# Optimization experiments

Hardware: AMD Instinct MI355X
Metric: run time of the kernel (lower is better)

Reference implementation:

```python
import jax, jax.numpy as jnp
import numpy as np

G, N, H, OUT, L = 16, 96, 128, 1, 3
DEG = 16
E = G * N * DEG


def setup_inputs() -> dict:
    key = jax.random.key(0)
    ks = iter(jax.random.split(key, 64))
    x = jax.random.randint(next(ks), (G * N, 9), 0, 2)
    edge_attr = jax.random.randint(next(ks), (E, 3), 0, 2)
    # edges grouped per graph (matches PyG batching); global node ids
    edge_graph = jnp.repeat(jnp.arange(G), E // G)
    edge_src = edge_graph * N + jax.random.randint(next(ks), (E,), 0, N)
    edge_dst = edge_graph * N + jax.random.randint(next(ks), (E,), 0, N)

    def lin(shape, fan_in):
        return jax.random.normal(next(ks), shape, jnp.float32) / np.sqrt(fan_in)

    return dict(
        x=x, edge_attr=edge_attr, edge_src=edge_src, edge_dst=edge_dst,
        num_graphs=G, max_nodes=N,
        atom_tables=jax.random.normal(next(ks), (9, 119, H)) * 0.02,
        bond_tables=jax.random.normal(next(ks), (3, 6, H)) * 0.02,
        W_m1=lin((L, 2, 2 * H, H), 2 * H), b_m1=jnp.zeros((L, 2, H)),
        W_m2=lin((L, 2, 2 * H, H), 2 * H), b_m2=jnp.zeros((L, 2, H)),
        W_me=lin((L, 2, H, H), H), b_me=jnp.zeros((L, 2, H)),
        W_mg=lin((L, 2, H, H), H), b_mg=jnp.zeros((L, 2, H)),
        W_mlp1=lin((L, 2, H, H), H), b_mlp1=jnp.zeros((L, 2, H)),
        W_mlp2=lin((L, 2, H, H), H), b_mlp2=jnp.zeros((L, 2, H)),
        W_o1=lin((L, 2, 2 * H, H), 2 * H), b_o1=jnp.zeros((L, 2, H)),
        W_o2=lin((L, 2, H, H), H), b_o2=jnp.zeros((L, 2, H)),
        ln_g=jnp.ones((L, 2, H)), ln_b=jnp.zeros((L, 2, H)),
        W_red=lin((L, 2 * H, H), 2 * H), b_red=jnp.zeros((L, H)),
        W_p1=lin((H, H), H), b_p1=jnp.zeros((H,)),
        W_p2=lin((H, OUT), H), b_p2=jnp.zeros((OUT,)),
    )


def _forward(x, edge_attr, edge_src, edge_dst, num_graphs, max_nodes,
             atom_tables, bond_tables, W_m1, b_m1, W_m2, b_m2, W_me, b_me,
             W_mg, b_mg, W_mlp1, b_mlp1, W_mlp2, b_mlp2, W_o1, b_o1,
             W_o2, b_o2, ln_g, ln_b, W_red, b_red, W_p1, b_p1, W_p2, b_p2):
    Hd = atom_tables.shape[-1]
    # OGB encoders: sum of per-column embeddings
    node_fts = atom_tables[jnp.arange(9)[:, None], x.T].sum(0)          # [G*N, H]
    edge_fts = bond_tables[jnp.arange(3)[:, None], edge_attr.T].sum(0)  # [E, H]
    node = node_fts.reshape(num_graphs, max_nodes, Hd)                  # to_dense_batch (equal-size graphs)
    # per-graph localization of global edge ids (== subtracting per-graph min)
    g = edge_src // max_nodes
    li = edge_src % max_nodes
    lj = edge_dst % max_nodes
    edge_dense = jnp.zeros((num_graphs, max_nodes, max_nodes, Hd),
                           node.dtype).at[g, li, lj].set(edge_fts)      # [G,N,N,H]
    graph_fts = jnp.zeros((num_graphs, Hd), node.dtype)
    hidden = jnp.zeros_like(node)
    for i in range(W_m1.shape[0]):
        outs = []
        for s in range(2):  # random / pretrained streams
            z = jnp.concatenate([node, hidden], -1)                     # [G,N,2H]
            msg1 = z @ W_m1[i, s] + b_m1[i, s]                          # [G,N,H]
            msg2 = z @ W_m2[i, s] + b_m2[i, s]
            msge = edge_dense @ W_me[i, s] + b_me[i, s]                 # [G,N,N,H]
            msgg = graph_fts @ W_mg[i, s] + b_mg[i, s]                  # [G,H]
            msgs = (msg1[:, None, :, :] + msg2[:, :, None, :]
                    + msge + msgg[:, None, None, :])
            m = jax.nn.relu(msgs)
            m = jax.nn.relu(m @ W_mlp1[i, s] + b_mlp1[i, s])
            msgs = m @ W_mlp2[i, s] + b_mlp2[i, s]
            # adj_mat is all ones -> masked max reduces to plain max over senders
            msgs = msgs.max(axis=1)                                     # [G,N,H]
            ret = z @ W_o1[i, s] + b_o1[i, s] + msgs @ W_o2[i, s] + b_o2[i, s]
            ret = jax.nn.relu(ret)
            mu = ret.mean(-1, keepdims=True)
            var = jnp.mean((ret - mu) ** 2, -1, keepdims=True)
            ret = (ret - mu) / jnp.sqrt(var + 1e-5) * ln_g[i, s] + ln_b[i, s]
            outs.append(ret)
        hidden = jnp.concatenate(outs, -1) @ W_red[i] + b_red[i]
    emb = hidden.mean(1)                                                # [G,H]
    h = jax.nn.relu(emb @ W_p1 + b_p1)
    return h @ W_p2 + b_p2                                              # [G,OUT]


def reference(x, edge_attr, edge_src, edge_dst, num_graphs, max_nodes,
              atom_tables, bond_tables, W_m1, b_m1, W_m2, b_m2, W_me, b_me,
              W_mg, b_mg, W_mlp1, b_mlp1, W_mlp2, b_mlp2, W_o1, b_o1,
              W_o2, b_o2, ln_g, ln_b, W_red, b_red, W_p1, b_p1, W_p2, b_p2):
    return _forward(x, edge_attr, edge_src, edge_dst, num_graphs, max_nodes,
                    atom_tables, bond_tables, W_m1, b_m1, W_m2, b_m2, W_me, b_me,
                    W_mg, b_mg, W_mlp1, b_mlp1, W_mlp2, b_mlp2, W_o1, b_o1,
                    W_o2, b_o2, ln_g, ln_b, W_red, b_red, W_p1, b_p1, W_p2, b_p2)
```

## Files before the change

### kernel.cpp

```cpp
#include <hip/hip_runtime.h>
#include <cstddef>

typedef _Float16 f16;
typedef f16 f16x8 __attribute__((ext_vector_type(8)));
typedef f16 f16x4 __attribute__((ext_vector_type(4)));
typedef float f32x4 __attribute__((ext_vector_type(4)));

constexpr int NG    = 16;
constexpr int NNODE = 96;
constexpr int TOTN  = 1536;
constexpr int HD    = 128;
constexpr int NEDGE = 24576;
constexpr int NLAY  = 3;
constexpr int NREG  = NG * 6 * 4;
constexpr int EMCAP = 128;
constexpr int EMSTR = 136;

__device__ __forceinline__ f32x4 mfma16(f16x8 a, f16x8 b, f32x4 c) {
    return __builtin_amdgcn_mfma_f32_16x16x32_f16(a, b, c, 0, 0, 0);
}

__global__ void k_embed_nodes(const int* x, const float* atab, f16* zA) {
    const int v = blockIdx.x, h = threadIdx.x;
    float s = 0.f;
    for (int c = 0; c < 9; ++c)
        s += atab[((size_t)(c * 119 + x[v * 9 + c])) * HD + h];
    const size_t base = ((size_t)(v >> 4) * 32);
    zA[((base + (h >> 3)) * 16 + (v & 15)) * 8 + (h & 7)] = (f16)s;
    zA[((base + 16 + (h >> 3)) * 16 + (v & 15)) * 8 + (h & 7)] = (f16)0.f;
}

__global__ void k_embed_edges(const int* ea, const float* btab, f16* eftsA) {
    const int e = blockIdx.x, h = threadIdx.x;
    float s = 0.f;
    for (int c = 0; c < 3; ++c)
        s += btab[((size_t)(c * 6 + ea[e * 3 + c])) * HD + h];
    eftsA[(((size_t)(e >> 4) * 16 + (h >> 3)) * 16 + (e & 15)) * 8 + (h & 7)] = (f16)s;
}

__global__ void k_init(int* winner, int* winner2, int* eperm, int* cnt) {
    const int idx = blockIdx.x * 256 + threadIdx.x;
    if (idx < NG * NNODE * NNODE) {
        winner[idx] = -1;
        winner2[idx] = -1;
    }
    if (idx < NEDGE) eperm[idx] = -1;
    if (idx < NREG) cnt[idx] = 0;
}

__global__ void k_winner(const int* esrc, const int* edst, int* winner) {
    const int e = blockIdx.x * 256 + threadIdx.x;
    const int sg = esrc[e];
    const int g = sg / NNODE;
    const int li = sg - g * NNODE;
    const int lj = edst[e] - g * NNODE;
    atomicMax(&winner[((size_t)g * NNODE + li) * NNODE + lj], e);
}

__device__ __forceinline__ int region_of(int idx) {
    const int b = idx / (NNODE * NNODE);
    const int r = idx - b * NNODE * NNODE;
    const int i = r / NNODE, j = r - (r / NNODE) * NNODE;
    return b * 24 + (j >> 4) * 4 + (i / 24);
}

__global__ void k_count(const int* winner, int* cnt) {
    const int idx = blockIdx.x * 256 + threadIdx.x;
    if (idx < NG * NNODE * NNODE && winner[idx] >= 0)
        atomicAdd(&cnt[region_of(idx)], 1);
}

__global__ void k_scan(const int* cnt, int* base, int* base0) {
    __shared__ int tmp[NREG];
    const int t = threadIdx.x;
    tmp[t] = cnt[t];
    __syncthreads();
    for (int off = 1; off < NREG; off <<= 1) {
        int v = (t >= off) ? tmp[t - off] : 0;
        __syncthreads();
        tmp[t] += v;
        __syncthreads();
    }
    const int ex = tmp[t] - cnt[t];
    base[t] = ex;
    base0[t] = ex;
}

__global__ void k_assign(const int* winner, int* base, int* winner2, int* eperm) {
    const int idx = blockIdx.x * 256 + threadIdx.x;
    if (idx >= NG * NNODE * NNODE) return;
    const int e = winner[idx];
    if (e >= 0) {
        const int p = atomicAdd(&base[region_of(idx)], 1);
        winner2[idx] = p;
        eperm[e] = p;
    }
}

__global__ void k_wswz(const float* Wm1, const float* Wm2, const float* Wo1,
                       const float* Wred, const float* Wo2, const float* W1,
                       const float* W2, const float* We,
                       f16* sm1, f16* sm2, f16* so1, f16* sred, f16* so2,
                       f16* s1, f16* s2, f16* sme) {
    const int idx = blockIdx.x * 256 + threadIdx.x;
    const int S256 = 6 * 256 * 128;
    const int SRED = 3 * 256 * 128;
    const int S128 = 6 * 128 * 128;
    const float* src;
    f16* dst;
    int rel, sh;
    if (idx < S256)                   { src = Wm1;  dst = sm1;  rel = idx;              sh = 15; }
    else if (idx < 2 * S256)          { src = Wm2;  dst = sm2;  rel = idx - S256;       sh = 15; }
    else if (idx < 3 * S256)          { src = Wo1;  dst = so1;  rel = idx - 2 * S256;   sh = 15; }
    else if (idx < 3 * S256 + SRED)   { src = Wred; dst = sred; rel = idx - 3 * S256;   sh = 15; }
    else if (idx < 3 * S256 + SRED + S128)
        { src = Wo2; dst = so2; rel = idx - 3 * S256 - SRED; sh = 14; }
    else if (idx < 3 * S256 + SRED + 2 * S128)
        { src = W1;  dst = s1;  rel = idx - 3 * S256 - SRED - S128; sh = 14; }
    else if (idx < 3 * S256 + SRED + 3 * S128)
        { src = W2;  dst = s2;  rel = idx - 3 * S256 - SRED - 2 * S128; sh = 14; }
    else if (idx < 3 * S256 + SRED + 4 * S128)
        { src = We;  dst = sme; rel = idx - 3 * S256 - SRED - 3 * S128; sh = 14; }
    else return;
    const int mat = rel >> sh;
    const int r2 = rel & ((1 << sh) - 1);
    const int k = r2 >> 7, n = r2 & 127;
    dst[(size_t)mat * (1 << sh) + (((k >> 3) * 128 + n) << 3) + (k & 7)] = (f16)src[rel];
}

__global__ __launch_bounds__(256) void k_ngemm(
    const f16* __restrict__ zA,
    const f16* __restrict__ sm1, const f16* __restrict__ sm2, const f16* __restrict__ so1,
    const float* __restrict__ bm1, const float* __restrict__ bm2,
    const float* __restrict__ bme, const float* __restrict__ bmg,
    const float* __restrict__ bo1,
    float* __restrict__ msg1, float* __restrict__ msg2, float* __restrict__ o1buf,
    int layer) {
    const int tid = threadIdx.x, lane = tid & 63, w = tid >> 6;
    const int mr = lane & 15, q = lane >> 4;
    const int t0 = blockIdx.x;
    const int wh = blockIdx.y >> 1, s = blockIdx.y & 1, ls = layer * 2 + s;
    const f16* B;
    float* out;
    float bias[8];
    if (wh == 0) {
        B = sm1 + (size_t)ls * 32768; out = msg1 + (size_t)s * TOTN * HD;
        for (int nt = 0; nt < 8; ++nt) {
            const int col = nt * 16 + mr;
            bias[nt] = bm1[ls * HD + col] + bme[ls * HD + col] + bmg[ls * HD + col];
        }
    } else if (wh == 1) {
        B = sm2 + (size_t)ls * 32768; out = msg2 + (size_t)s * TOTN * HD;
        for (int nt = 0; nt < 8; ++nt) bias[nt] = bm2[ls * HD + nt * 16 + mr];
    } else {
        B = so1 + (size_t)ls * 32768; out = o1buf + (size_t)s * TOTN * HD;
        for (int nt = 0; nt < 8; ++nt) bias[nt] = bo1[ls * HD + nt * 16 + mr];
    }
    const size_t tIdx = (size_t)t0 * 4 + w;
    f32x4 acc[8];
#pragma unroll
    for (int nt = 0; nt < 8; ++nt) acc[nt] = (f32x4){0.f, 0.f, 0.f, 0.f};
#pragma unroll
    for (int kt = 0; kt < 8; ++kt) {
        const int kq = kt * 4 + q;
        f16x8 a = *(const f16x8*)&zA[((tIdx * 32 + kq) * 16 + mr) * 8];
        const f16* bp = B + ((size_t)kq * HD) * 8;
#pragma unroll
        for (int nt = 0; nt < 8; ++nt) {
            f16x8 bv = *(const f16x8*)(bp + (nt * 16 + mr) * 8);
            acc[nt] = mfma16(a, bv, acc[nt]);
        }
    }
#pragma unroll
    for (int nt = 0; nt < 8; ++nt) {
        const int col = nt * 16 + mr;
#pragma unroll
        for (int r = 0; r < 4; ++r) {
            const int row = t0 * 64 + w * 16 + q * 4 + r;
            out[(size_t)row * HD + col] = acc[nt][r] + bias[nt];
        }
    }
}

__global__ __launch_bounds__(256) void k_egemm(
    const f16* __restrict__ eftsA, const f16* __restrict__ sme,
    const int* __restrict__ eperm, f16* __restrict__ emsgP) {
    const int tid = threadIdx.x, lane = tid & 63, w = tid >> 6;
    const int mr = lane & 15, q = lane >> 4;
    const int ls = blockIdx.y;
    const f16* B = sme + (size_t)ls * 16384;
    f32x4 acc[2][8];
#pragma unroll
    for (int mt = 0; mt < 2; ++mt)
#pragma unroll
        for (int nt = 0; nt < 8; ++nt) acc[mt][nt] = (f32x4){0.f, 0.f, 0.f, 0.f};
#pragma unroll
    for (int kt = 0; kt < 4; ++kt) {
        const int kq = kt * 4 + q;
        f16x8 a0 = *(const f16x8*)&eftsA[(((size_t)(blockIdx.x * 8 + 2 * w + 0) * 16 + kq) * 16 + mr) * 8];
        f16x8 a1 = *(const f16x8*)&eftsA[(((size_t)(blockIdx.x * 8 + 2 * w + 1) * 16 + kq) * 16 + mr) * 8];
        const f16* bp = B + ((size_t)kq * HD) * 8;
#pragma unroll
        for (int nt = 0; nt < 8; ++nt) {
            f16x8 bv = *(const f16x8*)(bp + (nt * 16 + mr) * 8);
            acc[0][nt] = mfma16(a0, bv, acc[0][nt]);
            acc[1][nt] = mfma16(a1, bv, acc[1][nt]);
        }
    }
#pragma unroll
    for (int mt = 0; mt < 2; ++mt) {
        const int ebase = blockIdx.x * 128 + (2 * w + mt) * 16 + q * 4;
#pragma unroll
        for (int r = 0; r < 4; ++r) {
            const int p = eperm[ebase + r];
            if (p < 0) continue;
            f16* orow = emsgP + ((size_t)ls * NEDGE + p) * HD;
#pragma unroll
            for (int nt = 0; nt < 8; ++nt)
                orow[nt * 16 + mr] = (f16)acc[mt][nt][r];
        }
    }
}

__global__ __launch_bounds__(256) void k_pairs(
    const float* __restrict__ msg1, const float* __restrict__ msg2,
    const f16* __restrict__ emsgP, const int* __restrict__ winner2,
    const int* __restrict__ cnt0, const int* __restrict__ base0,
    const f16* __restrict__ w1s, const float* __restrict__ bmlp1,
    const f16* __restrict__ w2s, const float* __restrict__ bmlp2,
    float* __restrict__ maxpart, int layer) {
    __shared__ __align__(16) f16 M2s[24 * 128];
    __shared__ __align__(16) f16 Qb[128 * 128];
    __shared__ __align__(16) f16 EMs[EMCAP * EMSTR];
    const int tid = threadIdx.x, lane = tid & 63, w = tid >> 6;
    const int mr = lane & 15, q = lane >> 4;
    const int jt = blockIdx.x, b = blockIdx.y, zz = blockIdx.z;
    const int cp = zz >> 1, s = zz & 1, ls = layer * 2 + s;
    const int j0 = jt * 16, i0 = cp * 24;
    const f16* EM = emsgP + (size_t)ls * NEDGE * HD;
    const f16* W1 = w1s + (size_t)ls * HD * HD;
    const f16* W2 = w2s + (size_t)ls * HD * HD;
    const int reg = b * 24 + jt * 4 + cp;
    const int rbase = base0[reg];
    const int rcnt = cnt0[reg];
    {
        const int lim = (rcnt < EMCAP ? rcnt : EMCAP) * 16;
        for (int idx = tid; idx < lim; idx += 256) {
            const int row = idx >> 4, seg = idx & 15;
            *(f16x8*)&EMs[row * EMSTR + seg * 8] =
                *(const f16x8*)&EM[((size_t)(rbase + row)) * HD + seg * 8];
        }
    }
    for (int idx = tid * 4; idx < 24 * 128; idx += 1024) {
        const int row = idx >> 7, col = idx & 127;
        float4 v = *(const float4*)&msg2[((size_t)s * TOTN + b * NNODE + i0 + row) * HD + col];
        f16x4 h;
        h[0] = (f16)v.x; h[1] = (f16)v.y; h[2] = (f16)v.z; h[3] = (f16)v.w;
        *(f16x4*)&M2s[idx] = h;
    }
    f16x8 m1f[4];
    {
        const float* m1p = msg1 + ((size_t)s * TOTN + b * NNODE + j0 + mr) * HD;
#pragma unroll
        for (int kt = 0; kt < 4; ++kt) {
            float4 p0 = *(const float4*)(m1p + kt * 32 + q * 8);
            float4 p1 = *(const float4*)(m1p + kt * 32 + q * 8 + 4);
            m1f[kt][0] = (f16)p0.x; m1f[kt][1] = (f16)p0.y;
            m1f[kt][2] = (f16)p0.z; m1f[kt][3] = (f16)p0.w;
            m1f[kt][4] = (f16)p1.x; m1f[kt][5] = (f16)p1.y;
            m1f[kt][6] = (f16)p1.z; m1f[kt][7] = (f16)p1.w;
        }
    }
    f16x8 Bf1[4][2], Bf2[4][2];
#pragma unroll
    for (int kt = 0; kt < 4; ++kt)
#pragma unroll
        for (int ntl = 0; ntl < 2; ++ntl) {
            const size_t off = ((size_t)(kt * 4 + q) * 128 + (2 * w + ntl) * 16 + mr) * 8;
            Bf1[kt][ntl] = *(const f16x8*)(W1 + off);
            Bf2[kt][ntl] = *(const f16x8*)(W2 + off);
        }
    float b1v[2], b2v[2];
#pragma unroll
    for (int ntl = 0; ntl < 2; ++ntl) {
        const int col = (2 * w + ntl) * 16 + mr;
        b1v[ntl] = bmlp1[ls * HD + col];
        b2v[ntl] = bmlp2[ls * HD + col];
    }
    float maxr[2][4];
#pragma unroll
    for (int ntl = 0; ntl < 2; ++ntl)
#pragma unroll
        for (int r = 0; r < 4; ++r) maxr[ntl][r] = -3.402823466e38f;
    __syncthreads();

    for (int it = 0; it < 3; ++it) {
        const int ibase = i0 + it * 8;
        int wv[8];
#pragma unroll
        for (int mt = 0; mt < 8; ++mt)
            wv[mt] = winner2[((size_t)b * NNODE + ibase + mt) * NNODE + j0 + mr];
        f32x4 acc[8][2];
#pragma unroll
        for (int mt = 0; mt < 8; ++mt)
#pragma unroll
            for (int ntl = 0; ntl < 2; ++ntl) acc[mt][ntl] = (f32x4){0.f, 0.f, 0.f, 0.f};
#pragma unroll
        for (int kt = 0; kt < 4; ++kt) {
            const int ko = kt * 32 + q * 8;
#pragma unroll
            for (int mt = 0; mt < 8; ++mt) {
                f16x8 m2v = *(const f16x8*)&M2s[(it * 8 + mt) * 128 + ko];
                f16x8 av = m1f[kt] + m2v;
                if (wv[mt] >= 0) {
                    const int lp = wv[mt] - rbase;
                    const f16* ep = (lp < EMCAP) ? &EMs[lp * EMSTR + ko]
                                                 : &EM[(size_t)wv[mt] * HD + ko];
                    f16x8 ev = *(const f16x8*)ep;
                    av = av + ev;
                }
#pragma unroll
                for (int u = 0; u < 8; ++u)
                    av[u] = av[u] > (f16)0.f ? av[u] : (f16)0.f;
                acc[mt][0] = mfma16(av, Bf1[kt][0], acc[mt][0]);
                acc[mt][1] = mfma16(av, Bf1[kt][1], acc[mt][1]);
            }
        }
#pragma unroll
        for (int mt = 0; mt < 8; ++mt)
#pragma unroll
            for (int ntl = 0; ntl < 2; ++ntl) {
                const int col = (2 * w + ntl) * 16 + mr;
                const int kg = col >> 3, kj = col & 7;
#pragma unroll
                for (int r = 0; r < 4; ++r) {
                    float v = fmaxf(acc[mt][ntl][r] + b1v[ntl], 0.f);
                    Qb[((mt * 16 + kg) * 16 + q * 4 + r) * 8 + kj] = (f16)v;
                }
            }
        __syncthreads();
#pragma unroll
        for (int mt = 0; mt < 8; ++mt)
#pragma unroll
            for (int ntl = 0; ntl < 2; ++ntl) acc[mt][ntl] = (f32x4){0.f, 0.f, 0.f, 0.f};
#pragma unroll
        for (int kt = 0; kt < 4; ++kt) {
#pragma unroll
            for (int mt = 0; mt < 8; ++mt) {
                f16x8 a = *(const f16x8*)&Qb[((mt * 16 + kt * 4 + q) * 16 + mr) * 8];
                acc[mt][0] = mfma16(a, Bf2[kt][0], acc[mt][0]);
                acc[mt][1] = mfma16(a, Bf2[kt][1], acc[mt][1]);
            }
        }
#pragma unroll
        for (int ntl = 0; ntl < 2; ++ntl)
#pragma unroll
            for (int r = 0; r < 4; ++r) {
                float m0 = acc[0][ntl][r];
#pragma unroll
                for (int mt = 1; mt < 8; ++mt) m0 = fmaxf(m0, acc[mt][ntl][r]);
                maxr[ntl][r] = fmaxf(maxr[ntl][r], m0 + b2v[ntl]);
            }
        __syncthreads();
    }
#pragma unroll
    for (int ntl = 0; ntl < 2; ++ntl) {
        const int col = (2 * w + ntl) * 16 + mr;
#pragma unroll
        for (int r = 0; r < 4; ++r) {
            const int j = j0 + q * 4 + r;
            maxpart[((size_t)zz * TOTN + b * NNODE + j) * HD + col] = maxr[ntl][r];
        }
    }
}

__global__ __launch_bounds__(256) void k_pr(
    const float* __restrict__ maxpart, const float* __restrict__ o1buf,
    const f16* __restrict__ so2, const float* __restrict__ bo2,
    const float* __restrict__ lng, const float* __restrict__ lnb,
    const f16* __restrict__ sred, const float* __restrict__ bred,
    float* __restrict__ hiddenf, f16* __restrict__ zA, int layer) {
    __shared__ __align__(16) f16 Af[16384];
    const int tid = threadIdx.x, lane = tid & 63, w = tid >> 6;
    const int mr = lane & 15, q = lane >> 4;
    const int row0 = blockIdx.x * 64;
    {
        const int mrow = tid >> 1, half = tid & 1;
        const int sb = mrow >> 6, rl = mrow & 63;
        const int row = row0 + rl;
#pragma unroll
        for (int c8 = 0; c8 < 64; c8 += 8) {
            const int col = half * 64 + c8;
            float mx[8] = {-3.4e38f, -3.4e38f, -3.4e38f, -3.4e38f,
                           -3.4e38f, -3.4e38f, -3.4e38f, -3.4e38f};
#pragma unroll
            for (int ch = 0; ch < 4; ++ch) {
                const float* p = maxpart + ((size_t)(ch * 2 + sb) * TOTN + row) * HD + col;
                float4 u0 = *(const float4*)p;
                float4 u1 = *(const float4*)(p + 4);
                mx[0] = fmaxf(mx[0], u0.x); mx[1] = fmaxf(mx[1], u0.y);
                mx[2] = fmaxf(mx[2], u0.z); mx[3] = fmaxf(mx[3], u0.w);
                mx[4] = fmaxf(mx[4], u1.x); mx[5] = fmaxf(mx[5], u1.y);
                mx[6] = fmaxf(mx[6], u1.z); mx[7] = fmaxf(mx[7], u1.w);
            }
            f16x8 pv;
#pragma unroll
            for (int u = 0; u < 8; ++u) pv[u] = (f16)mx[u];
            *(f16x8*)&Af[(((sb * 4 + (rl >> 4)) * 16 + (col >> 3)) * 16 + (rl & 15)) * 8] = pv;
        }
    }
    __syncthreads();
    const int sw = w >> 1, ls = layer * 2 + sw;
    const f16* B1 = so2 + (size_t)ls * 16384;
    f32x4 acc[2][8];
#pragma unroll
    for (int mt = 0; mt < 2; ++mt)
#pragma unroll
        for (int nt = 0; nt < 8; ++nt) acc[mt][nt] = (f32x4){0.f, 0.f, 0.f, 0.f};
#pragma unroll
    for (int kt = 0; kt < 4; ++kt) {
        const int kq = kt * 4 + q;
        f16x8 a0 = *(const f16x8*)&Af[(((sw * 4 + (w & 1) * 2 + 0) * 16 + kq) * 16 + mr) * 8];
        f16x8 a1 = *(const f16x8*)&Af[(((sw * 4 + (w & 1) * 2 + 1) * 16 + kq) * 16 + mr) * 8];
        const f16* bp = B1 + ((size_t)kq * HD) * 8;
#pragma unroll
        for (int nt = 0; nt < 8; ++nt) {
            f16x8 bv = *(const f16x8*)(bp + (nt * 16 + mr) * 8);
            acc[0][nt] = mfma16(a0, bv, acc[0][nt]);
            acc[1][nt] = mfma16(a1, bv, acc[1][nt]);
        }
    }
    float lngv[8], lnbv[8], bo2v[8];
#pragma unroll
    for (int nt = 0; nt < 8; ++nt) {
        const int col = nt * 16 + mr;
        lngv[nt] = lng[ls * HD + col];
        lnbv[nt] = lnb[ls * HD + col];
        bo2v[nt] = bo2[ls * HD + col];
    }
#pragma unroll
    for (int mt = 0; mt < 2; ++mt) {
#pragma unroll
        for (int nt = 0; nt < 8; ++nt) {
            const int col = nt * 16 + mr;
#pragma unroll
            for (int r = 0; r < 4; ++r) {
                const int rl = (w & 1) * 32 + mt * 16 + q * 4 + r;
                float v = acc[mt][nt][r] + bo2v[nt] +
                          o1buf[((size_t)sw * TOTN + row0 + rl) * HD + col];
                acc[mt][nt][r] = fmaxf(v, 0.f);
            }
        }
#pragma unroll
        for (int r = 0; r < 4; ++r) {
            float su = 0.f, sq = 0.f;
#pragma unroll
            for (int nt = 0; nt < 8; ++nt) {
                su += acc[mt][nt][r];
                sq += acc[mt][nt][r] * acc[mt][nt][r];
            }
#pragma unroll
            for (int mask = 1; mask <= 8; mask <<= 1) {
                su += __shfl_xor(su, mask, 64);
                sq += __shfl_xor(sq, mask, 64);
            }
            const float mean = su * (1.f / 128.f);
            float var = sq * (1.f / 128.f) - mean * mean;
            var = fmaxf(var, 0.f);
            const float rstd = 1.f / sqrtf(var + 1e-5f);
#pragma unroll
            for (int nt = 0; nt < 8; ++nt)
                acc[mt][nt][r] = (acc[mt][nt][r] - mean) * rstd * lngv[nt] + lnbv[nt];
        }
    }
    __syncthreads();
#pragma unroll
    for (int mt = 0; mt < 2; ++mt)
#pragma unroll
        for (int nt = 0; nt < 8; ++nt) {
            const int kg2 = sw * 16 + nt * 2 + (mr >> 3), j2 = mr & 7;
#pragma unroll
            for (int r = 0; r < 4; ++r) {
                const int rl = (w & 1) * 32 + mt * 16 + q * 4 + r;
                Af[(((rl >> 4) * 32 + kg2) * 16 + (rl & 15)) * 8 + j2] = (f16)acc[mt][nt][r];
            }
        }
    __syncthreads();
    const f16* B2 = sred + (size_t)layer * 32768;
    f32x4 a2[8];
#pragma unroll
    for (int nt = 0; nt < 8; ++nt) a2[nt] = (f32x4){0.f, 0.f, 0.f, 0.f};
#pragma unroll
    for (int kt = 0; kt < 8; ++kt) {
        const int kq = kt * 4 + q;
        f16x8 av = *(const f16x8*)&Af[((w * 32 + kq) * 16 + mr) * 8];
        const f16* bp = B2 + ((size_t)kq * HD) * 8;
#pragma unroll
        for (int nt = 0; nt < 8; ++nt) {
            f16x8 bv = *(const f16x8*)(bp + (nt * 16 + mr) * 8);
            a2[nt] = mfma16(av, bv, a2[nt]);
        }
    }
#pragma unroll
    for (int nt = 0; nt < 8; ++nt) {
        const int col = nt * 16 + mr;
        const float bb = bred[layer * HD + col];
#pragma unroll
        for (int r = 0; r < 4; ++r) {
            const int row = row0 + w * 16 + q * 4 + r;
            const float v = a2[nt][r] + bb;
            hiddenf[(size_t)row * HD + col] = v;
            zA[(((size_t)(row >> 4) * 32 + 16 + (col >> 3)) * 16 + (row & 15)) * 8 + (col & 7)] = (f16)v;
        }
    }
}

__global__ void k_final(const float* hiddenf, const float* Wp1, const float* bp1,
                        const float* Wp2, const float* bp2, float* out) {
    __shared__ float se[128];
    __shared__ float sr[128];
    const int b = blockIdx.x, h = threadIdx.x;
    float acc = 0.f;
    for (int v = 0; v < NNODE; ++v)
        acc += hiddenf[((size_t)b * NNODE + v) * HD + h];
    se[h] = acc * (1.f / 96.f);
    __syncthreads();
    float a2 = bp1[h];
    for (int k = 0; k < 128; ++k)
        a2 += se[k] * Wp1[(size_t)k * HD + h];
    a2 = fmaxf(a2, 0.f);
    sr[h] = a2 * Wp2[h];
    __syncthreads();
    for (int off = 64; off > 0; off >>= 1) {
        if (h < off) sr[h] += sr[h + off];
        __syncthreads();
    }
    if (h == 0) out[b] = sr[0] + bp2[0];
}

extern "C" void kernel_launch(void* const* d_in, const int* in_sizes, int n_in,
                              void* d_out, int out_size, void* d_ws, size_t ws_size,
                              hipStream_t stream) {
    (void)in_sizes; (void)n_in; (void)out_size; (void)ws_size;
    const int* x    = (const int*)d_in[0];
    const int* ea   = (const int*)d_in[1];
    const int* esrc = (const int*)d_in[2];
    const int* edst = (const int*)d_in[3];
    const float* atab = (const float*)d_in[6];
    const float* btab = (const float*)d_in[7];
    const float* Wm1 = (const float*)d_in[8];    const float* bm1 = (const float*)d_in[9];
    const float* Wm2 = (const float*)d_in[10];   const float* bm2 = (const float*)d_in[11];
    const float* Wme = (const float*)d_in[12];   const float* bme = (const float*)d_in[13];
    const float* bmg = (const float*)d_in[15];
    const float* Wmlp1 = (const float*)d_in[16]; const float* bmlp1 = (const float*)d_in[17];
    const float* Wmlp2 = (const float*)d_in[18]; const float* bmlp2 = (const float*)d_in[19];
    const float* Wo1 = (const float*)d_in[20];   const float* bo1 = (const float*)d_in[21];
    const float* Wo2 = (const float*)d_in[22];   const float* bo2 = (const float*)d_in[23];
    const float* lng = (const float*)d_in[24];   const float* lnb = (const float*)d_in[25];
    const float* Wred = (const float*)d_in[26];  const float* bred = (const float*)d_in[27];
    const float* Wp1 = (const float*)d_in[28];   const float* bp1 = (const float*)d_in[29];
    const float* Wp2 = (const float*)d_in[30];   const float* bp2 = (const float*)d_in[31];

    char* cur = (char*)d_ws;
    f16* zA = (f16*)cur;          cur += (size_t)TOTN * 256 * 2;
    float* hiddenf = (float*)cur; cur += (size_t)TOTN * HD * 4;
    f16* eftsA = (f16*)cur;       cur += (size_t)NEDGE * HD * 2;
    f16* emsgP = (f16*)cur;       cur += (size_t)6 * NEDGE * HD * 2;
    float* msg1 = (float*)cur;    cur += (size_t)2 * TOTN * HD * 4;
    float* msg2 = (float*)cur;    cur += (size_t)2 * TOTN * HD * 4;
    float* o1buf = (float*)cur;   cur += (size_t)2 * TOTN * HD * 4;
    float* maxpart = (float*)cur; cur += (size_t)8 * TOTN * HD * 4;
    int* winner = (int*)cur;      cur += (size_t)NG * NNODE * NNODE * 4;
    int* winner2 = (int*)cur;     cur += (size_t)NG * NNODE * NNODE * 4;
    int* eperm = (int*)cur;       cur += (size_t)NEDGE * 4;
    int* cnt = (int*)cur;         cur += (size_t)NREG * 4;
    int* basep = (int*)cur;       cur += (size_t)NREG * 4;
    int* base0 = (int*)cur;       cur += (size_t)NREG * 4;
    f16* sw1 = (f16*)cur;         cur += (size_t)6 * HD * HD * 2;
    f16* sw2 = (f16*)cur;         cur += (size_t)6 * HD * HD * 2;
    f16* swme = (f16*)cur;        cur += (size_t)6 * HD * HD * 2;
    f16* swm1 = (f16*)cur;        cur += (size_t)6 * 256 * HD * 2;
    f16* swm2 = (f16*)cur;        cur += (size_t)6 * 256 * HD * 2;
    f16* swo1 = (f16*)cur;        cur += (size_t)6 * 256 * HD * 2;
    f16* swred = (f16*)cur;       cur += (size_t)3 * 256 * HD * 2;
    f16* swo2 = (f16*)cur;        cur += (size_t)6 * HD * HD * 2;

    const int NPAIR = NG * NNODE * NNODE;
    k_init<<<(NPAIR + 255) / 256, 256, 0, stream>>>(winner, winner2, eperm, cnt);
    k_embed_nodes<<<TOTN, 128, 0, stream>>>(x, atab, zA);
    k_embed_edges<<<NEDGE, 128, 0, stream>>>(ea, btab, eftsA);
    k_winner<<<NEDGE / 256, 256, 0, stream>>>(esrc, edst, winner);
    k_count<<<(NPAIR + 255) / 256, 256, 0, stream>>>(winner, cnt);
    k_scan<<<1, NREG, 0, stream>>>(cnt, basep, base0);
    k_assign<<<(NPAIR + 255) / 256, 256, 0, stream>>>(winner, basep, winner2, eperm);
    k_wswz<<<4224, 256, 0, stream>>>(Wm1, Wm2, Wo1, Wred, Wo2, Wmlp1, Wmlp2, Wme,
                                     swm1, swm2, swo1, swred, swo2, sw1, sw2, swme);
    k_egemm<<<dim3(192, 6), 256, 0, stream>>>(eftsA, swme, eperm, emsgP);
    for (int layer = 0; layer < NLAY; ++layer) {
        k_ngemm<<<dim3(24, 6), 256, 0, stream>>>(zA, swm1, swm2, swo1,
                                                 bm1, bm2, bme, bmg, bo1,
                                                 msg1, msg2, o1buf, layer);
        k_pairs<<<dim3(6, NG, 8), 256, 0, stream>>>(msg1, msg2, emsgP, winner2,
                                                    cnt, base0,
                                                    sw1, bmlp1, sw2, bmlp2,
                                                    maxpart, layer);
        k_pr<<<24, 256, 0, stream>>>(maxpart, o1buf, swo2, bo2, lng, lnb,
                                     swred, bred, hiddenf, zA, layer);
    }
    k_final<<<NG, 128, 0, stream>>>(hiddenf, Wp1, bp1, Wp2, bp2, (float*)d_out);
}
```

Before: 505.7 us.

## Split pair kernel into finer i-chunks, store max partials in fp16, fuse prep kernels

The pairs kernel now handles 8 source rows per block instead of 24, so the grid grows from 8 to 24 z-slices and there are more concurrent blocks. Each block also needs less shared memory and fewer registers, since it no longer loops over three i-chunks or preloads the W2 fragments. Max partials are written as fp16 and reduced over 12 chunks in k_pr, which halves the bytes per partial but triples the number of partials. The init, embedding and weight-swizzle launches are merged into a single prep kernel to cut launch overhead. The costs are more redundant loads of W1, msg1 and the edge messages across blocks, and an fp16 max-reduction in place of fp32.

```diff
diff --git a/kernel.cpp b/kernel.cpp
--- a/kernel.cpp
+++ b/kernel.cpp
@@ -12,107 +12,59 @@
 constexpr int HD    = 128;
 constexpr int NEDGE = 24576;
 constexpr int NLAY  = 3;
-constexpr int NREG  = NG * 6 * 4;
-constexpr int EMCAP = 128;
-constexpr int EMSTR = 136;
+constexpr int NPAIR = NG * NNODE * NNODE;
+constexpr int NREG  = NG * 6 * 12;
+constexpr int EMCAP = 64;
+constexpr int EMSTR = 132;
 
 __device__ __forceinline__ f32x4 mfma16(f16x8 a, f16x8 b, f32x4 c) {
     return __builtin_amdgcn_mfma_f32_16x16x32_f16(a, b, c, 0, 0, 0);
 }
 
-__global__ void k_embed_nodes(const int* x, const float* atab, f16* zA) {
-    const int v = blockIdx.x, h = threadIdx.x;
-    float s = 0.f;
-    for (int c = 0; c < 9; ++c)
-        s += atab[((size_t)(c * 119 + x[v * 9 + c])) * HD + h];
-    const size_t base = ((size_t)(v >> 4) * 32);
-    zA[((base + (h >> 3)) * 16 + (v & 15)) * 8 + (h & 7)] = (f16)s;
-    zA[((base + 16 + (h >> 3)) * 16 + (v & 15)) * 8 + (h & 7)] = (f16)0.f;
-}
-
-__global__ void k_embed_edges(const int* ea, const float* btab, f16* eftsA) {
-    const int e = blockIdx.x, h = threadIdx.x;
-    float s = 0.f;
-    for (int c = 0; c < 3; ++c)
-        s += btab[((size_t)(c * 6 + ea[e * 3 + c])) * HD + h];
-    eftsA[(((size_t)(e >> 4) * 16 + (h >> 3)) * 16 + (e & 15)) * 8 + (h & 7)] = (f16)s;
-}
-
-__global__ void k_init(int* winner, int* winner2, int* eperm, int* cnt) {
-    const int idx = blockIdx.x * 256 + threadIdx.x;
-    if (idx < NG * NNODE * NNODE) {
-        winner[idx] = -1;
-        winner2[idx] = -1;
-    }
-    if (idx < NEDGE) eperm[idx] = -1;
-    if (idx < NREG) cnt[idx] = 0;
-}
-
-__global__ void k_winner(const int* esrc, const int* edst, int* winner) {
-    const int e = blockIdx.x * 256 + threadIdx.x;
-    const int sg = esrc[e];
-    const int g = sg / NNODE;
-    const int li = sg - g * NNODE;
-    const int lj = edst[e] - g * NNODE;
-    atomicMax(&winner[((size_t)g * NNODE + li) * NNODE + lj], e);
-}
-
-__device__ __forceinline__ int region_of(int idx) {
-    const int b = idx / (NNODE * NNODE);
-    const int r = idx - b * NNODE * NNODE;
-    const int i = r / NNODE, j = r - (r / NNODE) * NNODE;
-    return b * 24 + (j >> 4) * 4 + (i / 24);
-}
-
-__global__ void k_count(const int* winner, int* cnt) {
-    const int idx = blockIdx.x * 256 + threadIdx.x;
-    if (idx < NG * NNODE * NNODE && winner[idx] >= 0)
-        atomicAdd(&cnt[region_of(idx)], 1);
-}
-
-__global__ void k_scan(const int* cnt, int* base, int* base0) {
-    __shared__ int tmp[NREG];
-    const int t = threadIdx.x;
-    tmp[t] = cnt[t];
-    __syncthreads();
-    for (int off = 1; off < NREG; off <<= 1) {
-        int v = (t >= off) ? tmp[t - off] : 0;
-        __syncthreads();
-        tmp[t] += v;
-        __syncthreads();
-    }
-    const int ex = tmp[t] - cnt[t];
-    base[t] = ex;
-    base0[t] = ex;
-}
-
-__global__ void k_assign(const int* winner, int* base, int* winner2, int* eperm) {
-    const int idx = blockIdx.x * 256 + threadIdx.x;
-    if (idx >= NG * NNODE * NNODE) return;
-    const int e = winner[idx];
-    if (e >= 0) {
-        const int p = atomicAdd(&base[region_of(idx)], 1);
-        winner2[idx] = p;
-        eperm[e] = p;
-    }
-}
-
-__global__ void k_wswz(const float* Wm1, const float* Wm2, const float* Wo1,
-                       const float* Wred, const float* Wo2, const float* W1,
-                       const float* W2, const float* We,
-                       f16* sm1, f16* sm2, f16* so1, f16* sred, f16* so2,
-                       f16* s1, f16* s2, f16* sme) {
-    const int idx = blockIdx.x * 256 + threadIdx.x;
-    const int S256 = 6 * 256 * 128;
-    const int SRED = 3 * 256 * 128;
-    const int S128 = 6 * 128 * 128;
+__global__ __launch_bounds__(256) void k_prep(
+    const int* x, const float* atab, const int* ea, const float* btab,
+    const float* Wm1, const float* Wm2, const float* Wo1, const float* Wred,
+    const float* Wo2, const float* W1, const float* W2, const float* We,
+    f16* zA, f16* eftsA, int* winner, int* winner2, int* eperm, int* cnt,
+    f16* sm1, f16* sm2, f16* so1, f16* sred, f16* so2, f16* s1, f16* s2, f16* sme) {
+    const int blk = blockIdx.x, tid = threadIdx.x;
+    if (blk < 576) {
+        const int idx = blk * 256 + tid;
+        if (idx < NPAIR) {
+            winner[idx] = -1;
+            winner2[idx] = -1;
+        }
+        if (idx < NEDGE) eperm[idx] = -1;
+        if (idx < NREG) cnt[idx] = 0;
+        return;
+    }
+    if (blk < 576 + 768) {
+        const int v = (blk - 576) * 2 + (tid >> 7), h = tid & 127;
+        float s = 0.f;
+        for (int c = 0; c < 9; ++c)
+            s += atab[((size_t)(c * 119 + x[v * 9 + c])) * HD + h];
+        const size_t base = ((size_t)(v >> 4) * 32);
+        zA[((base + (h >> 3)) * 16 + (v & 15)) * 8 + (h & 7)] = (f16)s;
+        zA[((base + 16 + (h >> 3)) * 16 + (v & 15)) * 8 + (h & 7)] = (f16)0.f;
+        return;
+    }
+    if (blk < 576 + 768 + 12288) {
+        const int e = (blk - 576 - 768) * 2 + (tid >> 7), h = tid & 127;
+        float s = 0.f;
+        for (int c = 0; c < 3; ++c)
+            s += btab[((size_t)(c * 6 + ea[e * 3 + c])) * HD + h];
+        eftsA[(((size_t)(e >> 4) * 16 + (h >> 3)) * 16 + (e & 15)) * 8 + (h & 7)] = (f16)s;
+        return;
+    }
+    const int idx = (blk - 576 - 768 - 12288) * 256 + tid;
+    const int S256 = 6 * 256 * 128, SRED = 3 * 256 * 128, S128 = 6 * 128 * 128;
     const float* src;
     f16* dst;
     int rel, sh;
-    if (idx < S256)                   { src = Wm1;  dst = sm1;  rel = idx;              sh = 15; }
-    else if (idx < 2 * S256)          { src = Wm2;  dst = sm2;  rel = idx - S256;       sh = 15; }
-    else if (idx < 3 * S256)          { src = Wo1;  dst = so1;  rel = idx - 2 * S256;   sh = 15; }
-    else if (idx < 3 * S256 + SRED)   { src = Wred; dst = sred; rel = idx - 3 * S256;   sh = 15; }
+    if (idx < S256)                 { src = Wm1;  dst = sm1;  rel = idx;            sh = 15; }
+    else if (idx < 2 * S256)        { src = Wm2;  dst = sm2;  rel = idx - S256;     sh = 15; }
+    else if (idx < 3 * S256)        { src = Wo1;  dst = so1;  rel = idx - 2 * S256; sh = 15; }
+    else if (idx < 3 * S256 + SRED) { src = Wred; dst = sred; rel = idx - 3 * S256; sh = 15; }
     else if (idx < 3 * S256 + SRED + S128)
         { src = Wo2; dst = so2; rel = idx - 3 * S256 - SRED; sh = 14; }
     else if (idx < 3 * S256 + SRED + 2 * S128)
@@ -126,6 +78,56 @@
     const int r2 = rel & ((1 << sh) - 1);
     const int k = r2 >> 7, n = r2 & 127;
     dst[(size_t)mat * (1 << sh) + (((k >> 3) * 128 + n) << 3) + (k & 7)] = (f16)src[rel];
+}
+
+__global__ void k_winner(const int* esrc, const int* edst, int* winner) {
+    const int e = blockIdx.x * 256 + threadIdx.x;
+    const int sg = esrc[e];
+    const int g = sg / NNODE;
+    const int li = sg - g * NNODE;
+    const int lj = edst[e] - g * NNODE;
+    atomicMax(&winner[((size_t)g * NNODE + li) * NNODE + lj], e);
+}
+
+__device__ __forceinline__ int region_of(int idx) {
+    const int b = idx / (NNODE * NNODE);
+    const int r = idx - b * NNODE * NNODE;
+    const int i = r / NNODE, j = r - (r / NNODE) * NNODE;
+    return b * 72 + (j >> 4) * 12 + (i >> 3);
+}
+
+__global__ void k_count(const int* winner, int* cnt) {
+    const int idx = blockIdx.x * 256 + threadIdx.x;
+    if (idx < NPAIR && winner[idx] >= 0)
+        atomicAdd(&cnt[region_of(idx)], 1);
+}
+
+__global__ void k_scan(const int* cnt, int* base, int* base0) {
+    __shared__ int tmp[576];
+    const int t = threadIdx.x;
+    const int c0 = cnt[2 * t], c1 = cnt[2 * t + 1];
+    tmp[t] = c0 + c1;
+    __syncthreads();
+    for (int off = 1; off < 576; off <<= 1) {
+        int v = (t >= off) ? tmp[t - off] : 0;
+        __syncthreads();
+        tmp[t] += v;
+        __syncthreads();
+    }
+    const int ex = tmp[t] - (c0 + c1);
+    base[2 * t] = ex;          base0[2 * t] = ex;
+    base[2 * t + 1] = ex + c0; base0[2 * t + 1] = ex + c0;
+}
+
+__global__ void k_assign(const int* winner, int* base, int* winner2, int* eperm) {
+    const int idx = blockIdx.x * 256 + threadIdx.x;
+    if (idx >= NPAIR) return;
+    const int e = winner[idx];
+    if (e >= 0) {
+        const int p = atomicAdd(&base[region_of(idx)], 1);
+        winner2[idx] = p;
+        eperm[e] = p;
+    }
 }
 
 __global__ __launch_bounds__(256) void k_ngemm(
@@ -228,19 +230,19 @@
     const int* __restrict__ cnt0, const int* __restrict__ base0,
     const f16* __restrict__ w1s, const float* __restrict__ bmlp1,
     const f16* __restrict__ w2s, const float* __restrict__ bmlp2,
-    float* __restrict__ maxpart, int layer) {
-    __shared__ __align__(16) f16 M2s[24 * 128];
+    f16* __restrict__ maxpart, int layer) {
+    __shared__ __align__(16) f16 EMs[EMCAP * EMSTR];
+    __shared__ __align__(16) f16 M2s[8 * 128];
     __shared__ __align__(16) f16 Qb[128 * 128];
-    __shared__ __align__(16) f16 EMs[EMCAP * EMSTR];
     const int tid = threadIdx.x, lane = tid & 63, w = tid >> 6;
     const int mr = lane & 15, q = lane >> 4;
     const int jt = blockIdx.x, b = blockIdx.y, zz = blockIdx.z;
     const int cp = zz >> 1, s = zz & 1, ls = layer * 2 + s;
-    const int j0 = jt * 16, i0 = cp * 24;
+    const int j0 = jt * 16, i0 = cp * 8;
     const f16* EM = emsgP + (size_t)ls * NEDGE * HD;
     const f16* W1 = w1s + (size_t)ls * HD * HD;
     const f16* W2 = w2s + (size_t)ls * HD * HD;
-    const int reg = b * 24 + jt * 4 + cp;
+    const int reg = b * 72 + jt * 12 + cp;
     const int rbase = base0[reg];
     const int rcnt = cnt0[reg];
     {
@@ -251,12 +253,12 @@
                 *(const f16x8*)&EM[((size_t)(rbase + row)) * HD + seg * 8];
         }
     }
-    for (int idx = tid * 4; idx < 24 * 128; idx += 1024) {
-        const int row = idx >> 7, col = idx & 127;
-        float4 v = *(const float4*)&msg2[((size_t)s * TOTN + b * NNODE + i0 + row) * HD + col];
+    {
+        const int row = tid >> 5, c4 = (tid & 31) * 4;
+        float4 v = *(const float4*)&msg2[((size_t)s * TOTN + b * NNODE + i0 + row) * HD + c4];
         f16x4 h;
         h[0] = (f16)v.x; h[1] = (f16)v.y; h[2] = (f16)v.z; h[3] = (f16)v.w;
-        *(f16x4*)&M2s[idx] = h;
+        *(f16x4*)&M2s[row * 128 + c4] = h;
     }
     f16x8 m1f[4];
     {
@@ -271,15 +273,13 @@
             m1f[kt][6] = (f16)p1.z; m1f[kt][7] = (f16)p1.w;
         }
     }
-    f16x8 Bf1[4][2], Bf2[4][2];
+    f16x8 Bf1[4][2];
 #pragma unroll
     for (int kt = 0; kt < 4; ++kt)
 #pragma unroll
-        for (int ntl = 0; ntl < 2; ++ntl) {
-            const size_t off = ((size_t)(kt * 4 + q) * 128 + (2 * w + ntl) * 16 + mr) * 8;
-            Bf1[kt][ntl] = *(const f16x8*)(W1 + off);
-            Bf2[kt][ntl] = *(const f16x8*)(W2 + off);
-        }
+        for (int ntl = 0; ntl < 2; ++ntl)
+            Bf1[kt][ntl] = *(const f16x8*)(W1 +
+                ((size_t)(kt * 4 + q) * 128 + (2 * w + ntl) * 16 + mr) * 8);
     float b1v[2], b2v[2];
 #pragma unroll
     for (int ntl = 0; ntl < 2; ++ntl) {
@@ -287,95 +287,81 @@
         b1v[ntl] = bmlp1[ls * HD + col];
         b2v[ntl] = bmlp2[ls * HD + col];
     }
-    float maxr[2][4];
-#pragma unroll
-    for (int ntl = 0; ntl < 2; ++ntl)
-#pragma unroll
-        for (int r = 0; r < 4; ++r) maxr[ntl][r] = -3.402823466e38f;
-    __syncthreads();
-
-    for (int it = 0; it < 3; ++it) {
-        const int ibase = i0 + it * 8;
-        int wv[8];
-#pragma unroll
-        for (int mt = 0; mt < 8; ++mt)
-            wv[mt] = winner2[((size_t)b * NNODE + ibase + mt) * NNODE + j0 + mr];
-        f32x4 acc[8][2];
-#pragma unroll
-        for (int mt = 0; mt < 8; ++mt)
-#pragma unroll
-            for (int ntl = 0; ntl < 2; ++ntl) acc[mt][ntl] = (f32x4){0.f, 0.f, 0.f, 0.f};
-#pragma unroll
-        for (int kt = 0; kt < 4; ++kt) {
-            const int ko = kt * 32 + q * 8;
-#pragma unroll
-            for (int mt = 0; mt < 8; ++mt) {
-                f16x8 m2v = *(const f16x8*)&M2s[(it * 8 + mt) * 128 + ko];
-                f16x8 av = m1f[kt] + m2v;
-                if (wv[mt] >= 0) {
-                    const int lp = wv[mt] - rbase;
-                    const f16* ep = (lp < EMCAP) ? &EMs[lp * EMSTR + ko]
-                                                 : &EM[(size_t)wv[mt] * HD + ko];
-                    f16x8 ev = *(const f16x8*)ep;
-                    av = av + ev;
-                }
-#pragma unroll
-                for (int u = 0; u < 8; ++u)
-                    av[u] = av[u] > (f16)0.f ? av[u] : (f16)0.f;
-                acc[mt][0] = mfma16(av, Bf1[kt][0], acc[mt][0]);
-                acc[mt][1] = mfma16(av, Bf1[kt][1], acc[mt][1]);
-            }
-        }
-#pragma unroll
-        for (int mt = 0; mt < 8; ++mt)
-#pragma unroll
-            for (int ntl = 0; ntl < 2; ++ntl) {
-                const int col = (2 * w + ntl) * 16 + mr;
-                const int kg = col >> 3, kj = col & 7;
-#pragma unroll
-                for (int r = 0; r < 4; ++r) {
-                    float v = fmaxf(acc[mt][ntl][r] + b1v[ntl], 0.f);
-                    Qb[((mt * 16 + kg) * 16 + q * 4 + r) * 8 + kj] = (f16)v;
-                }
-            }
-        __syncthreads();
-#pragma unroll
-        for (int mt = 0; mt < 8; ++mt)
-#pragma unroll
-            for (int ntl = 0; ntl < 2; ++ntl) acc[mt][ntl] = (f32x4){0.f, 0.f, 0.f, 0.f};
-#pragma unroll
-        for (int kt = 0; kt < 4; ++kt) {
-#pragma unroll
-            for (int mt = 0; mt < 8; ++mt) {
-                f16x8 a = *(const f16x8*)&Qb[((mt * 16 + kt * 4 + q) * 16 + mr) * 8];
-                acc[mt][0] = mfma16(a, Bf2[kt][0], acc[mt][0]);
-                acc[mt][1] = mfma16(a, Bf2[kt][1], acc[mt][1]);
-            }
-        }
-#pragma unroll
-        for (int ntl = 0; ntl < 2; ++ntl)
+    int wv[8];
+#pragma unroll
+    for (int mt = 0; mt < 8; ++mt)
+        wv[mt] = winner2[((size_t)b * NNODE + i0 + mt) * NNODE + j0 + mr];
+    __syncthreads();
+    f32x4 acc[8][2];
+#pragma unroll
+    for (int mt = 0; mt < 8; ++mt)
+#pragma unroll
+        for (int ntl = 0; ntl < 2; ++ntl) acc[mt][ntl] = (f32x4){0.f, 0.f, 0.f, 0.f};
+#pragma unroll
+    for (int kt = 0; kt < 4; ++kt) {
+        const int ko = kt * 32 + q * 8;
+#pragma unroll
+        for (int mt = 0; mt < 8; ++mt) {
+            f16x8 m2v = *(const f16x8*)&M2s[mt * 128 + ko];
+            f16x8 av = m1f[kt] + m2v;
+            if (wv[mt] >= 0) {
+                const int lp = wv[mt] - rbase;
+                f16x8 ev;
+                if (lp < EMCAP) ev = *(const f16x8*)&EMs[lp * EMSTR + ko];
+                else            ev = *(const f16x8*)&EM[(size_t)wv[mt] * HD + ko];
+                av = av + ev;
+            }
+#pragma unroll
+            for (int u = 0; u < 8; ++u)
+                av[u] = av[u] > (f16)0.f ? av[u] : (f16)0.f;
+            acc[mt][0] = mfma16(av, Bf1[kt][0], acc[mt][0]);
+            acc[mt][1] = mfma16(av, Bf1[kt][1], acc[mt][1]);
+        }
+    }
+#pragma unroll
+    for (int mt = 0; mt < 8; ++mt)
+#pragma unroll
+        for (int ntl = 0; ntl < 2; ++ntl) {
+            const int col = (2 * w + ntl) * 16 + mr;
+            const int kg = col >> 3, kj = col & 7;
 #pragma unroll
             for (int r = 0; r < 4; ++r) {
-                float m0 = acc[0][ntl][r];
-#pragma unroll
-                for (int mt = 1; mt < 8; ++mt) m0 = fmaxf(m0, acc[mt][ntl][r]);
-                maxr[ntl][r] = fmaxf(maxr[ntl][r], m0 + b2v[ntl]);
-            }
-        __syncthreads();
+                float v = fmaxf(acc[mt][ntl][r] + b1v[ntl], 0.f);
+                Qb[((mt * 16 + kg) * 16 + q * 4 + r) * 8 + kj] = (f16)v;
+            }
+        }
+    __syncthreads();
+#pragma unroll
+    for (int mt = 0; mt < 8; ++mt)
+#pragma unroll
+        for (int ntl = 0; ntl < 2; ++ntl) acc[mt][ntl] = (f32x4){0.f, 0.f, 0.f, 0.f};
+#pragma unroll
+    for (int kt = 0; kt < 4; ++kt) {
+        f16x8 bv0 = *(const f16x8*)(W2 + ((size_t)(kt * 4 + q) * 128 + (2 * w + 0) * 16 + mr) * 8);
+        f16x8 bv1 = *(const f16x8*)(W2 + ((size_t)(kt * 4 + q) * 128 + (2 * w + 1) * 16 + mr) * 8);
+#pragma unroll
+        for (int mt = 0; mt < 8; ++mt) {
+            f16x8 a = *(const f16x8*)&Qb[((mt * 16 + kt * 4 + q) * 16 + mr) * 8];
+            acc[mt][0] = mfma16(a, bv0, acc[mt][0]);
+            acc[mt][1] = mfma16(a, bv1, acc[mt][1]);
+        }
     }
 #pragma unroll
     for (int ntl = 0; ntl < 2; ++ntl) {
         const int col = (2 * w + ntl) * 16 + mr;
 #pragma unroll
         for (int r = 0; r < 4; ++r) {
+            float m0 = acc[0][ntl][r];
+#pragma unroll
+            for (int mt = 1; mt < 8; ++mt) m0 = fmaxf(m0, acc[mt][ntl][r]);
             const int j = j0 + q * 4 + r;
-            maxpart[((size_t)zz * TOTN + b * NNODE + j) * HD + col] = maxr[ntl][r];
+            maxpart[((size_t)zz * TOTN + b * NNODE + j) * HD + col] = (f16)(m0 + b2v[ntl]);
         }
     }
 }
 
 __global__ __launch_bounds__(256) void k_pr(
-    const float* __restrict__ maxpart, const float* __restrict__ o1buf,
+    const f16* __restrict__ maxpart, const float* __restrict__ o1buf,
     const f16* __restrict__ so2, const float* __restrict__ bo2,
     const float* __restrict__ lng, const float* __restrict__ lnb,
     const f16* __restrict__ sred, const float* __restrict__ bred,
@@ -391,22 +377,14 @@
 #pragma unroll
         for (int c8 = 0; c8 < 64; c8 += 8) {
             const int col = half * 64 + c8;
-            float mx[8] = {-3.4e38f, -3.4e38f, -3.4e38f, -3.4e38f,
-                           -3.4e38f, -3.4e38f, -3.4e38f, -3.4e38f};
-#pragma unroll
-            for (int ch = 0; ch < 4; ++ch) {
-                const float* p = maxpart + ((size_t)(ch * 2 + sb) * TOTN + row) * HD + col;
-                float4 u0 = *(const float4*)p;
-                float4 u1 = *(const float4*)(p + 4);
-                mx[0] = fmaxf(mx[0], u0.x); mx[1] = fmaxf(mx[1], u0.y);
-                mx[2] = fmaxf(mx[2], u0.z); mx[3] = fmaxf(mx[3], u0.w);
-                mx[4] = fmaxf(mx[4], u1.x); mx[5] = fmaxf(mx[5], u1.y);
-                mx[6] = fmaxf(mx[6], u1.z); mx[7] = fmaxf(mx[7], u1.w);
-            }
-            f16x8 pv;
-#pragma unroll
-            for (int u = 0; u < 8; ++u) pv[u] = (f16)mx[u];
-            *(f16x8*)&Af[(((sb * 4 + (rl >> 4)) * 16 + (col >> 3)) * 16 + (rl & 15)) * 8] = pv;
+            f16x8 mx = *(const f16x8*)&maxpart[((size_t)(0 * 2 + sb) * TOTN + row) * HD + col];
+#pragma unroll
+            for (int cp = 1; cp < 12; ++cp) {
+                f16x8 v = *(const f16x8*)&maxpart[((size_t)(cp * 2 + sb) * TOTN + row) * HD + col];
+#pragma unroll
+                for (int u = 0; u < 8; ++u) mx[u] = mx[u] > v[u] ? mx[u] : v[u];
+            }
+            *(f16x8*)&Af[(((sb * 4 + (rl >> 4)) * 16 + (col >> 3)) * 16 + (rl & 15)) * 8] = mx;
         }
     }
     __syncthreads();
@@ -569,9 +547,9 @@
     float* msg1 = (float*)cur;    cur += (size_t)2 * TOTN * HD * 4;
     float* msg2 = (float*)cur;    cur += (size_t)2 * TOTN * HD * 4;
     float* o1buf = (float*)cur;   cur += (size_t)2 * TOTN * HD * 4;
-    float* maxpart = (float*)cur; cur += (size_t)8 * TOTN * HD * 4;
-    int* winner = (int*)cur;      cur += (size_t)NG * NNODE * NNODE * 4;
-    int* winner2 = (int*)cur;     cur += (size_t)NG * NNODE * NNODE * 4;
+    f16* maxpart = (f16*)cur;     cur += (size_t)24 * TOTN * HD * 2;
+    int* winner = (int*)cur;      cur += (size_t)NPAIR * 4;
+    int* winner2 = (int*)cur;     cur += (size_t)NPAIR * 4;
     int* eperm = (int*)cur;       cur += (size_t)NEDGE * 4;
     int* cnt = (int*)cur;         cur += (size_t)NREG * 4;
     int* basep = (int*)cur;       cur += (size_t)NREG * 4;
@@ -585,25 +563,23 @@
     f16* swred = (f16*)cur;       cur += (size_t)3 * 256 * HD * 2;
     f16* swo2 = (f16*)cur;        cur += (size_t)6 * HD * HD * 2;
 
-    const int NPAIR = NG * NNODE * NNODE;
-    k_init<<<(NPAIR + 255) / 256, 256, 0, stream>>>(winner, winner2, eperm, cnt);
-    k_embed_nodes<<<TOTN, 128, 0, stream>>>(x, atab, zA);
-    k_embed_edges<<<NEDGE, 128, 0, stream>>>(ea, btab, eftsA);
+    k_prep<<<576 + 768 + 12288 + 4224, 256, 0, stream>>>(
+        x, atab, ea, btab, Wm1, Wm2, Wo1, Wred, Wo2, Wmlp1, Wmlp2, Wme,
+        zA, eftsA, winner, winner2, eperm, cnt,
+        swm1, swm2, swo1, swred, swo2, sw1, sw2, swme);
     k_winner<<<NEDGE / 256, 256, 0, stream>>>(esrc, edst, winner);
     k_count<<<(NPAIR + 255) / 256, 256, 0, stream>>>(winner, cnt);
-    k_scan<<<1, NREG, 0, stream>>>(cnt, basep, base0);
+    k_scan<<<1, 576, 0, stream>>>(cnt, basep, base0);
     k_assign<<<(NPAIR + 255) / 256, 256, 0, stream>>>(winner, basep, winner2, eperm);
-    k_wswz<<<4224, 256, 0, stream>>>(Wm1, Wm2, Wo1, Wred, Wo2, Wmlp1, Wmlp2, Wme,
-                                     swm1, swm2, swo1, swred, swo2, sw1, sw2, swme);
     k_egemm<<<dim3(192, 6), 256, 0, stream>>>(eftsA, swme, eperm, emsgP);
     for (int layer = 0; layer < NLAY; ++layer) {
         k_ngemm<<<dim3(24, 6), 256, 0, stream>>>(zA, swm1, swm2, swo1,
                                                  bm1, bm2, bme, bmg, bo1,
                                                  msg1, msg2, o1buf, layer);
-        k_pairs<<<dim3(6, NG, 8), 256, 0, stream>>>(msg1, msg2, emsgP, winner2,
-                                                    cnt, base0,
-                                                    sw1, bmlp1, sw2, bmlp2,
-                                                    maxpart, layer);
+        k_pairs<<<dim3(6, NG, 24), 256, 0, stream>>>(msg1, msg2, emsgP, winner2,
+                                                     cnt, base0,
+                                                     sw1, bmlp1, sw2, bmlp2,
+                                                     maxpart, layer);
         k_pr<<<24, 256, 0, stream>>>(maxpart, o1buf, swo2, bo2, lng, lnb,
                                      swred, bred, hiddenf, zA, layer);
     }
```

Result: faster. 420.2 us (-16.9%).
